# Kernel optimization log

Measured on AMD Instinct MI355X. Metric: run time of the kernel, lower is better.

Reference implementation:

```python
import jax, jax.numpy as jnp
import numpy as np

B, LAT, ADIM, NACT, H = 131072, 64, 16, 9, 128

def setup_inputs() -> dict:
    key = jax.random.key(0)
    ks = jax.random.split(key, 24)
    p = lambda k, shp: (jax.random.normal(k, shp, dtype=jnp.float32) * 0.05)
    return {
        "z_t": jax.random.normal(ks[0], (B, LAT), dtype=jnp.float32),
        "action": jax.random.randint(ks[1], (B,), 0, NACT),
        "hidden": jnp.zeros((1, B, H), dtype=jnp.float32),
        "embed": p(ks[2], (NACT, ADIM)),
        "fuse_W": p(ks[3], (H, LAT + ADIM)), "fuse_b": p(ks[4], (H,)),
        "W_ih": p(ks[5], (3 * H, H)), "W_hh": p(ks[6], (3 * H, H)),
        "b_ih": p(ks[7], (3 * H,)), "b_hh": p(ks[8], (3 * H,)),
        "ns_W1": p(ks[9], (H, H)), "ns_b1": p(ks[10], (H,)),
        "ns_W2": p(ks[11], (LAT, H)), "ns_b2": p(ks[12], (LAT,)),
        "rw_W1": p(ks[13], (H // 2, H)), "rw_b1": p(ks[14], (H // 2,)),
        "rw_W2": p(ks[15], (1, H // 2)), "rw_b2": p(ks[16], (1,)),
        "dn_W1": p(ks[17], (H // 2, H)), "dn_b1": p(ks[18], (H // 2,)),
        "dn_W2": p(ks[19], (1, H // 2)), "dn_b2": p(ks[20], (1,)),
    }

def _mlp2(x, W1, b1, W2, b2):
    return jax.nn.relu(x @ W1.T + b1) @ W2.T + b2

def reference(z_t, action, hidden, embed, fuse_W, fuse_b, W_ih, W_hh, b_ih, b_hh,
              ns_W1, ns_b1, ns_W2, ns_b2, rw_W1, rw_b1, rw_W2, rw_b2,
              dn_W1, dn_b1, dn_W2, dn_b2):
    a_emb = embed[action]                                  # [B, ADIM]
    fused = jnp.concatenate([z_t, a_emb], axis=-1)         # [B, LAT+ADIM]
    x = jax.nn.relu(fused @ fuse_W.T + fuse_b)             # [B, H]
    h0 = hidden[0]                                         # [B, H]
    gi = x @ W_ih.T + b_ih                                 # [B, 3H]
    gh = h0 @ W_hh.T + b_hh                                # [B, 3H]
    Hd = x.shape[-1]
    r = jax.nn.sigmoid(gi[:, :Hd] + gh[:, :Hd])
    zg = jax.nn.sigmoid(gi[:, Hd:2 * Hd] + gh[:, Hd:2 * Hd])
    n = jnp.tanh(gi[:, 2 * Hd:] + r * gh[:, 2 * Hd:])
    h_new = (1.0 - zg) * n + zg * h0                       # [B, H]
    out = h_new
    z_next = _mlp2(out, ns_W1, ns_b1, ns_W2, ns_b2)        # [B, LAT]
    reward = _mlp2(out, rw_W1, rw_b1, rw_W2, rw_b2)        # [B, 1]
    done_logit = _mlp2(out, dn_W1, dn_b1, dn_W2, dn_b2)    # [B, 1]
    return (z_next, reward, done_logit, h_new[None])
```

## Files before the change

kernel.cpp:

```cpp
#include <hip/hip_runtime.h>
#include <hip/hip_bf16.h>
#include <cstddef>
#include <cstdint>

#define BATCH 131072
#define HOFF ((size_t)BATCH * 66)

typedef __attribute__((ext_vector_type(8))) short short8;
typedef __attribute__((ext_vector_type(4))) short short4v;
typedef __attribute__((ext_vector_type(4))) float f32x4;
typedef __attribute__((ext_vector_type(16))) float f32x16;

typedef const __attribute__((address_space(1))) unsigned int* gas_t;
typedef __attribute__((address_space(3))) unsigned int* las_t;

#define WS_G      13312
#define WS_HEAD   117760
#define WS_ELEMS  161280

#define SLOT_A    0
#define SLOT_B    8704
#define STR_BASE  17408

#define MFMA32(a,b,c) __builtin_amdgcn_mfma_f32_32x32x16_bf16((a),(b),(c),0,0,0)

__device__ __forceinline__ short f2bf(float x) {
    __hip_bfloat16 b = __float2bfloat16(x);
    return __builtin_bit_cast(short, b);
}
__device__ __forceinline__ float bf2f(short s) {
    unsigned u = ((unsigned)(unsigned short)s) << 16;
    return __builtin_bit_cast(float, u);
}
__device__ __forceinline__ float fsigmoid(float x) { return __builtin_amdgcn_rcpf(1.0f + __expf(-x)); }
__device__ __forceinline__ float ftanh(float x)    { return 1.0f - 2.0f * __builtin_amdgcn_rcpf(1.0f + __expf(2.0f * x)); }

__device__ __forceinline__ short8 packbf(f32x4 a, f32x4 b) {
    short8 r;
    r[0]=f2bf(a[0]); r[1]=f2bf(a[1]); r[2]=f2bf(a[2]); r[3]=f2bf(a[3]);
    r[4]=f2bf(b[0]); r[5]=f2bf(b[1]); r[6]=f2bf(b[2]); r[7]=f2bf(b[3]);
    return r;
}

template<int NCH>
__device__ __forceinline__ void stage_lds(const short* __restrict__ src, short* dst, int t) {
    constexpr int NP = (NCH + 255) / 256;
    #pragma unroll
    for (int k = 0; k < NP; ++k) {
        int c = t + 256 * k;
        if ((NCH % 256 == 0) || c < NCH)
            __builtin_amdgcn_global_load_lds((gas_t)(const void*)(src + (size_t)c * 8),
                                             (las_t)(void*)(dst + (size_t)c * 8), 16, 0, 0);
    }
}

extern "C" __global__ void prep_weights(const float* __restrict__ fuse_W,
                                        const float* __restrict__ W_ih, const float* __restrict__ W_hh,
                                        const float* __restrict__ ns_W1, const float* __restrict__ ns_W2,
                                        const float* __restrict__ rw_W1, const float* __restrict__ dn_W1,
                                        short* __restrict__ ws) {
    int i = blockIdx.x * 256 + threadIdx.x;
    if (i >= WS_ELEMS) return;
    float v = 0.f;
    if (i < WS_G) {
        int half = i / 6656, e = i % 6656;
        int r = e / 104, k = e % 104;
        if (k < 80) v = fuse_W[(size_t)(half*64 + r)*80 + k];
    } else if (i < WS_HEAD) {
        int rel = i - WS_G;
        int pidx = rel / 8704, e = rel % 8704;
        int q = e / 4352, r = (e % 4352) / 136, k = e % 136;
        if (k < 128) {
            int u = pidx / 3, p = pidx % 3;
            const float* W; int gate;
            if (p == 0)      { W = q ? W_hh : W_ih; gate = 0; }
            else if (p == 1) { W = q ? W_ih : W_hh; gate = 2; }
            else             { W = q ? W_hh : W_ih; gate = 1; }
            v = W[(size_t)(gate*128 + u*32 + r)*128 + k];
        }
    } else {
        int rel = i - WS_HEAD;
        int h = rel / 8704, e = rel % 8704;
        int q = e / 4352, r = (e % 4352) / 136, k = e % 136;
        if (k < 128) {
            const float* W; int rb;
            if (h == 0)      { W = ns_W1; rb = q*32; }
            else if (h == 1) { W = ns_W1; rb = 64 + q*32; }
            else if (h == 2) { W = ns_W2; rb = q*32; }
            else if (h == 3) { W = rw_W1; rb = q*32; }
            else             { W = dn_W1; rb = q*32; }
            v = W[(size_t)(rb + r)*128 + k];
        }
    }
    ws[i] = f2bf(v);
}

#define GRU_R(SB, U) do {                                                                  \
    *(short8*)&S[ln*40 + hb8]      = ha[2*(U)];                                            \
    *(short8*)&S[ln*40 + 16 + hb8] = ha[2*(U)+1];                                          \
    _Pragma("unroll") for (int p = 0; p < 8; ++p) {                                        \
        const int r0 = 2*p, r1 = 2*p + 1;                                                  \
        unsigned a = (unsigned short)S[((r0&3) + 8*(r0>>2) + hr4)*40 + ln];                \
        unsigned b = (unsigned short)S[((r1&3) + 8*(r1>>2) + hr4)*40 + ln];                \
        h0p[p] = a | (b << 16);                                                            \
    }                                                                                      \
    const int cb = (U)*32 + ln;                                                            \
    const float br = b_ih[cb] + b_hh[cb];                                                  \
    f32x16 acc = zz16;                                                                     \
    _Pragma("unroll") for (int kf = 0; kf < 8; ++kf) {                                     \
        const int ko = kf*16 + hb8;                                                        \
        short8 B0 = *(const short8*)&smem[(SB) + ln*136 + ko];                             \
        acc = MFMA32(xa[kf], B0, acc);                                                     \
        short8 B1 = *(const short8*)&smem[(SB) + (32 + ln)*136 + ko];                      \
        acc = MFMA32(ha[kf], B1, acc);                                                     \
    }                                                                                      \
    _Pragma("unroll") for (int reg = 0; reg < 16; ++reg)                                   \
        tmp[reg] = fsigmoid(acc[reg] + br);                                                \
} while (0)

#define GRU_N(SB, U) do {                                                                  \
    const int cb = (U)*32 + ln;                                                            \
    const float bin = b_ih[256 + cb], bhn = b_hh[256 + cb];                                \
    f32x16 acc = zz16;                                                                     \
    _Pragma("unroll") for (int kf = 0; kf < 8; ++kf) {                                     \
        short8 B = *(const short8*)&smem[(SB) + ln*136 + kf*16 + hb8];                     \
        acc = MFMA32(ha[kf], B, acc);                                                      \
    }                                                                                      \
    _Pragma("unroll") for (int reg = 0; reg < 16; ++reg)                                   \
        tmp[reg] = tmp[reg] * (acc[reg] + bhn);                                            \
    acc = zz16;                                                                            \
    _Pragma("unroll") for (int kf = 0; kf < 8; ++kf) {                                     \
        short8 B = *(const short8*)&smem[(SB) + (32 + ln)*136 + kf*16 + hb8];              \
        acc = MFMA32(xa[kf], B, acc);                                                      \
    }                                                                                      \
    _Pragma("unroll") for (int reg = 0; reg < 16; ++reg)                                   \
        tmp[reg] = ftanh(acc[reg] + bin + tmp[reg]);                                       \
} while (0)

#define GRU_Z(SB, U) do {                                                                  \
    const int cb = (U)*32 + ln;                                                            \
    const float bz = b_ih[128 + cb] + b_hh[128 + cb];                                      \
    f32x16 acc = zz16;                                                                     \
    _Pragma("unroll") for (int kf = 0; kf < 8; ++kf) {                                     \
        const int ko = kf*16 + hb8;                                                        \
        short8 B0 = *(const short8*)&smem[(SB) + ln*136 + ko];                             \
        acc = MFMA32(xa[kf], B0, acc);                                                     \
        short8 B1 = *(const short8*)&smem[(SB) + (32 + ln)*136 + ko];                      \
        acc = MFMA32(ha[kf], B1, acc);                                                     \
    }                                                                                      \
    _Pragma("unroll") for (int p = 0; p < 8; ++p) {                                        \
        unsigned hp = h0p[p];                                                              \
        _Pragma("unroll") for (int q = 0; q < 2; ++q) {                                    \
            const int reg = 2*p + q;                                                       \
            float h0v = bf2f((short)(q ? (hp >> 16) : (hp & 0xffffu)));                    \
            float zg = fsigmoid(acc[reg] + bz);                                            \
            S[((reg&3) + 8*(reg>>2) + hr4)*40 + ln] = f2bf((1.f - zg)*tmp[reg] + zg*h0v);  \
        }                                                                                  \
    }                                                                                      \
    hfa[2*(U)]   = *(const short8*)&S[ln*40 + hb8];                                        \
    hfa[2*(U)+1] = *(const short8*)&S[ln*40 + 16 + hb8];                                   \
    store_hnew(U);                                                                         \
} while (0)

#define HEAD32(FRAG, BIASEXPR, SB, Q, RELU) do {                                           \
    f32x16 a = zz16;                                                                       \
    _Pragma("unroll") for (int kf = 0; kf < 8; ++kf) {                                     \
        short8 B = *(const short8*)&smem[(SB) + (Q)*4352 + ln*136 + kf*16 + hb8];          \
        a = MFMA32((FRAG)[kf], B, a);                                                      \
    }                                                                                      \
    const float bb = (BIASEXPR);                                                           \
    _Pragma("unroll") for (int reg = 0; reg < 16; ++reg) {                                 \
        float v = a[reg] + bb;                                                             \
        if (RELU) v = fmaxf(v, 0.f);                                                       \
        S[((reg&3) + 8*(reg>>2) + hr4)*40 + ln] = f2bf(v);                                 \
    }                                                                                      \
} while (0)

extern "C" __global__ __launch_bounds__(256, 1)
void gru_mfma(const float* __restrict__ z_t, const int* __restrict__ action,
              const float* __restrict__ hidden, const float* __restrict__ embed,
              const float* __restrict__ fuse_b,
              const float* __restrict__ b_ih, const float* __restrict__ b_hh,
              const float* __restrict__ ns_b1, const float* __restrict__ ns_b2,
              const float* __restrict__ rw_b1, const float* __restrict__ rw_W2, const float* __restrict__ rw_b2,
              const float* __restrict__ dn_b1, const float* __restrict__ dn_W2, const float* __restrict__ dn_b2,
              const short* __restrict__ ws, float* out)
{
    __shared__ __align__(16) short smem[22528];

    const int t    = threadIdx.x;
    const int lane = t & 63;
    const int w    = t >> 6;
    const int ln   = lane & 31;
    const int hb8  = (lane >> 5) * 8;
    const int hr4  = (lane >> 5) * 4;
    const int R    = blockIdx.x * 128 + w * 32;
    short* const S = &smem[STR_BASE + w * 1280];

    const f32x16 zz16 = {0,0,0,0,0,0,0,0,0,0,0,0,0,0,0,0};

    auto store_hnew = [&](int j2) {
        #pragma unroll
        for (int v = 0; v < 4; ++v) {
            int idx = v*64 + lane;
            int r = idx >> 3, c = (idx & 7) * 4;
            short4v s = *(const short4v*)&S[r*40 + c];
            f32x4 f = { bf2f(s[0]), bf2f(s[1]), bf2f(s[2]), bf2f(s[3]) };
            *(f32x4*)&out[HOFF + (size_t)(R + r)*128 + j2*32 + c] = f;
        }
    };
    auto store_z = [&](int q) {
        #pragma unroll
        for (int v = 0; v < 4; ++v) {
            int idx = v*64 + lane;
            int r = idx >> 3, c = (idx & 7) * 4;
            short4v s = *(const short4v*)&S[r*40 + c];
            f32x4 f = { bf2f(s[0]), bf2f(s[1]), bf2f(s[2]), bf2f(s[3]) };
            *(f32x4*)&out[(size_t)(R + r)*64 + q*32 + c] = f;
        }
    };
    auto hpartial = [&](const float* W2, float acc) -> float {
        int rr = lane & 31;
        #pragma unroll
        for (int kk = 0; kk < 32; kk += 8) {
            short8 s = *(const short8*)&S[rr*40 + kk];
            f32x4 w0 = *(const f32x4*)&W2[kk];
            f32x4 w1 = *(const f32x4*)&W2[kk+4];
            acc += bf2f(s[0])*w0[0] + bf2f(s[1])*w0[1] + bf2f(s[2])*w0[2] + bf2f(s[3])*w0[3]
                 + bf2f(s[4])*w1[0] + bf2f(s[5])*w1[1] + bf2f(s[6])*w1[2] + bf2f(s[7])*w1[3];
        }
        return acc;
    };

    stage_lds<832>(ws, &smem[SLOT_A], t);

    short8 fa[5];
    short8 ha[8];
    {
        const int row = R + ln;
        #pragma unroll
        for (int kf = 0; kf < 4; ++kf) {
            f32x4 p0 = *(const f32x4*)&z_t[(size_t)row*64 + kf*16 + hb8];
            f32x4 p1 = *(const f32x4*)&z_t[(size_t)row*64 + kf*16 + hb8 + 4];
            fa[kf] = packbf(p0, p1);
        }
        int a = action[row];
        f32x4 e0 = *(const f32x4*)&embed[a*16 + hb8];
        f32x4 e1 = *(const f32x4*)&embed[a*16 + hb8 + 4];
        fa[4] = packbf(e0, e1);
        #pragma unroll
        for (int kf = 0; kf < 8; ++kf) {
            f32x4 p0 = *(const f32x4*)&hidden[(size_t)row*128 + kf*16 + hb8];
            f32x4 p1 = *(const f32x4*)&hidden[(size_t)row*128 + kf*16 + hb8 + 4];
            ha[kf] = packbf(p0, p1);
        }
    }

    short8 xa[8], hfa[8];
    f32x16 tmp;
    unsigned h0p[8];

    __syncthreads();
    stage_lds<832>(ws + 6656, &smem[SLOT_B], t);
    #pragma unroll
    for (int n = 0; n < 2; ++n) {
        f32x16 a = zz16;
        #pragma unroll
        for (int kf = 0; kf < 5; ++kf) {
            short8 B = *(const short8*)&smem[SLOT_A + (n*32 + ln)*104 + kf*16 + hb8];
            a = MFMA32(fa[kf], B, a);
        }
        float fb = fuse_b[n*32 + ln];
        #pragma unroll
        for (int reg = 0; reg < 16; ++reg)
            S[((reg&3) + 8*(reg>>2) + hr4)*40 + ln] = f2bf(fmaxf(a[reg] + fb, 0.f));
        xa[2*n]   = *(const short8*)&S[ln*40 + hb8];
        xa[2*n+1] = *(const short8*)&S[ln*40 + 16 + hb8];
    }

    __syncthreads();
    stage_lds<1088>(ws + WS_G + 0*8704, &smem[SLOT_A], t);
    #pragma unroll
    for (int n = 2; n < 4; ++n) {
        f32x16 a = zz16;
        #pragma unroll
        for (int kf = 0; kf < 5; ++kf) {
            short8 B = *(const short8*)&smem[SLOT_B + ((n-2)*32 + ln)*104 + kf*16 + hb8];
            a = MFMA32(fa[kf], B, a);
        }
        float fb = fuse_b[n*32 + ln];
        #pragma unroll
        for (int reg = 0; reg < 16; ++reg)
            S[((reg&3) + 8*(reg>>2) + hr4)*40 + ln] = f2bf(fmaxf(a[reg] + fb, 0.f));
        xa[2*n]   = *(const short8*)&S[ln*40 + hb8];
        xa[2*n+1] = *(const short8*)&S[ln*40 + 16 + hb8];
    }

    __syncthreads();
    stage_lds<1088>(ws + WS_G + 1*8704, &smem[SLOT_B], t);
    GRU_R(SLOT_A, 0);
    __syncthreads();
    stage_lds<1088>(ws + WS_G + 2*8704, &smem[SLOT_A], t);
    GRU_N(SLOT_B, 0);
    __syncthreads();
    stage_lds<1088>(ws + WS_G + 3*8704, &smem[SLOT_B], t);
    GRU_Z(SLOT_A, 0);
    __syncthreads();
    stage_lds<1088>(ws + WS_G + 4*8704, &smem[SLOT_A], t);
    GRU_R(SLOT_B, 1);
    __syncthreads();
    stage_lds<1088>(ws + WS_G + 5*8704, &smem[SLOT_B], t);
    GRU_N(SLOT_A, 1);
    __syncthreads();
    stage_lds<1088>(ws + WS_G + 6*8704, &smem[SLOT_A], t);
    GRU_Z(SLOT_B, 1);
    __syncthreads();
    stage_lds<1088>(ws + WS_G + 7*8704, &smem[SLOT_B], t);
    GRU_R(SLOT_A, 2);
    __syncthreads();
    stage_lds<1088>(ws + WS_G + 8*8704, &smem[SLOT_A], t);
    GRU_N(SLOT_B, 2);
    __syncthreads();
    stage_lds<1088>(ws + WS_G + 9*8704, &smem[SLOT_B], t);
    GRU_Z(SLOT_A, 2);
    __syncthreads();
    stage_lds<1088>(ws + WS_G + 10*8704, &smem[SLOT_A], t);
    GRU_R(SLOT_B, 3);
    __syncthreads();
    stage_lds<1088>(ws + WS_G + 11*8704, &smem[SLOT_B], t);
    GRU_N(SLOT_A, 3);
    __syncthreads();
    stage_lds<1088>(ws + WS_HEAD + 0*8704, &smem[SLOT_A], t);
    GRU_Z(SLOT_B, 3);

    short8 ta[8];
    __syncthreads();
    stage_lds<1088>(ws + WS_HEAD + 1*8704, &smem[SLOT_B], t);
    HEAD32(hfa, ns_b1[ln],      SLOT_A, 0, true);
    ta[0] = *(const short8*)&S[ln*40 + hb8];
    ta[1] = *(const short8*)&S[ln*40 + 16 + hb8];
    HEAD32(hfa, ns_b1[32 + ln], SLOT_A, 1, true);
    ta[2] = *(const short8*)&S[ln*40 + hb8];
    ta[3] = *(const short8*)&S[ln*40 + 16 + hb8];

    __syncthreads();
    stage_lds<1088>(ws + WS_HEAD + 2*8704, &smem[SLOT_A], t);
    HEAD32(hfa, ns_b1[64 + ln], SLOT_B, 0, true);
    ta[4] = *(const short8*)&S[ln*40 + hb8];
    ta[5] = *(const short8*)&S[ln*40 + 16 + hb8];
    HEAD32(hfa, ns_b1[96 + ln], SLOT_B, 1, true);
    ta[6] = *(const short8*)&S[ln*40 + hb8];
    ta[7] = *(const short8*)&S[ln*40 + 16 + hb8];

    __syncthreads();
    stage_lds<1088>(ws + WS_HEAD + 3*8704, &smem[SLOT_B], t);
    HEAD32(ta, ns_b2[ln],      SLOT_A, 0, false);
    store_z(0);
    HEAD32(ta, ns_b2[32 + ln], SLOT_A, 1, false);
    store_z(1);

    __syncthreads();
    stage_lds<1088>(ws + WS_HEAD + 4*8704, &smem[SLOT_A], t);
    float racc = rw_b2[0];
    HEAD32(hfa, rw_b1[ln],      SLOT_B, 0, true);
    racc = hpartial(rw_W2, racc);
    HEAD32(hfa, rw_b1[32 + ln], SLOT_B, 1, true);
    racc = hpartial(rw_W2 + 32, racc);
    if (lane < 32) out[(size_t)BATCH*64 + R + ln] = racc;

    __syncthreads();
    float dacc = dn_b2[0];
    HEAD32(hfa, dn_b1[ln],      SLOT_A, 0, true);
    dacc = hpartial(dn_W2, dacc);
    HEAD32(hfa, dn_b1[32 + ln], SLOT_A, 1, true);
    dacc = hpartial(dn_W2 + 32, dacc);
    if (lane < 32) out[(size_t)BATCH*65 + R + ln] = dacc;
}

extern "C" void kernel_launch(void* const* d_in, const int* in_sizes, int n_in,
                              void* d_out, int out_size, void* d_ws, size_t ws_size,
                              hipStream_t stream) {
    const float* z_t    = (const float*)d_in[0];
    const int*   action = (const int*)  d_in[1];
    const float* hidden = (const float*)d_in[2];
    const float* embed  = (const float*)d_in[3];
    const float* fuse_W = (const float*)d_in[4];
    const float* fuse_b = (const float*)d_in[5];
    const float* W_ih   = (const float*)d_in[6];
    const float* W_hh   = (const float*)d_in[7];
    const float* b_ih   = (const float*)d_in[8];
    const float* b_hh   = (const float*)d_in[9];
    const float* ns_W1  = (const float*)d_in[10];
    const float* ns_b1  = (const float*)d_in[11];
    const float* ns_W2  = (const float*)d_in[12];
    const float* ns_b2  = (const float*)d_in[13];
    const float* rw_W1  = (const float*)d_in[14];
    const float* rw_b1  = (const float*)d_in[15];
    const float* rw_W2  = (const float*)d_in[16];
    const float* rw_b2  = (const float*)d_in[17];
    const float* dn_W1  = (const float*)d_in[18];
    const float* dn_b1  = (const float*)d_in[19];
    const float* dn_W2  = (const float*)d_in[20];
    const float* dn_b2  = (const float*)d_in[21];
    float* out = (float*)d_out;
    short* ws  = (short*)d_ws;

    hipLaunchKernelGGL(prep_weights, dim3((WS_ELEMS + 255) / 256), dim3(256), 0, stream,
                       fuse_W, W_ih, W_hh, ns_W1, ns_W2, rw_W1, dn_W1, ws);

    hipLaunchKernelGGL(gru_mfma, dim3(BATCH / 128), dim3(256), 0, stream,
                       z_t, action, hidden, embed,
                       fuse_b, b_ih, b_hh, ns_b1, ns_b2,
                       rw_b1, rw_W2, rw_b2, dn_b1, dn_W2, dn_b2,
                       ws, out);
}
```

Measured before the change: 82.07 us.

## Write GRU outputs directly from MFMA accumulators and reload h_new via global

Removes the LDS transposes used for h0 extraction, h_new writeback and z_next writeback. h0 values are now read straight from global in the accumulator layout, and h_new and z_next are stored directly from accumulator registers as scalar strided stores. The bf16 operand fragments for the heads are rebuilt by reading h_new back from the output buffer. This cuts LDS traffic and register pressure from the held hfa fragments, but it trades vectorised stores for uncoalesced 4-byte stores and adds global re-reads. The readback also depends on same-thread write visibility, which holds only because each lane reads its own row region after a barrier.

```diff
diff --git a/kernel.cpp b/kernel.cpp
--- a/kernel.cpp
+++ b/kernel.cpp
@@ -96,15 +96,13 @@
 }
 
 #define GRU_R(SB, U) do {                                                                  \
-    *(short8*)&S[ln*40 + hb8]      = ha[2*(U)];                                            \
-    *(short8*)&S[ln*40 + 16 + hb8] = ha[2*(U)+1];                                          \
+    const int cb = (U)*32 + ln;                                                            \
     _Pragma("unroll") for (int p = 0; p < 8; ++p) {                                        \
-        const int r0 = 2*p, r1 = 2*p + 1;                                                  \
-        unsigned a = (unsigned short)S[((r0&3) + 8*(r0>>2) + hr4)*40 + ln];                \
-        unsigned b = (unsigned short)S[((r1&3) + 8*(r1>>2) + hr4)*40 + ln];                \
+        const int r0 = ((2*p)&3) + 8*(p>>1) + hr4;                                         \
+        unsigned a = (unsigned short)f2bf(hidden[(size_t)(R + r0    )*128 + cb]);          \
+        unsigned b = (unsigned short)f2bf(hidden[(size_t)(R + r0 + 1)*128 + cb]);          \
         h0p[p] = a | (b << 16);                                                            \
     }                                                                                      \
-    const int cb = (U)*32 + ln;                                                            \
     const float br = b_ih[cb] + b_hh[cb];                                                  \
     f32x16 acc = zz16;                                                                     \
     _Pragma("unroll") for (int kf = 0; kf < 8; ++kf) {                                     \
@@ -150,16 +148,14 @@
     }                                                                                      \
     _Pragma("unroll") for (int p = 0; p < 8; ++p) {                                        \
         unsigned hp = h0p[p];                                                              \
-        _Pragma("unroll") for (int q = 0; q < 2; ++q) {                                    \
-            const int reg = 2*p + q;                                                       \
-            float h0v = bf2f((short)(q ? (hp >> 16) : (hp & 0xffffu)));                    \
-            float zg = fsigmoid(acc[reg] + bz);                                            \
-            S[((reg&3) + 8*(reg>>2) + hr4)*40 + ln] = f2bf((1.f - zg)*tmp[reg] + zg*h0v);  \
-        }                                                                                  \
-    }                                                                                      \
-    hfa[2*(U)]   = *(const short8*)&S[ln*40 + hb8];                                        \
-    hfa[2*(U)+1] = *(const short8*)&S[ln*40 + 16 + hb8];                                   \
-    store_hnew(U);                                                                         \
+        const int r0 = ((2*p)&3) + 8*(p>>1) + hr4;                                         \
+        {   float h0v = bf2f((short)(hp & 0xffffu));                                       \
+            float zg = fsigmoid(acc[2*p] + bz);                                            \
+            out[HOFF + (size_t)(R + r0)*128 + cb] = (1.f - zg)*tmp[2*p] + zg*h0v; }        \
+        {   float h0v = bf2f((short)(hp >> 16));                                           \
+            float zg = fsigmoid(acc[2*p+1] + bz);                                          \
+            out[HOFF + (size_t)(R + r0 + 1)*128 + cb] = (1.f - zg)*tmp[2*p+1] + zg*h0v; }  \
+    }                                                                                      \
 } while (0)
 
 #define HEAD32(FRAG, BIASEXPR, SB, Q, RELU) do {                                           \
@@ -173,6 +169,19 @@
         float v = a[reg] + bb;                                                             \
         if (RELU) v = fmaxf(v, 0.f);                                                       \
         S[((reg&3) + 8*(reg>>2) + hr4)*40 + ln] = f2bf(v);                                 \
+    }                                                                                      \
+} while (0)
+
+#define HEAD32_ST(FRAG, BIASEXPR, SB, Q, QCOL) do {                                        \
+    f32x16 a = zz16;                                                                       \
+    _Pragma("unroll") for (int kf = 0; kf < 8; ++kf) {                                     \
+        short8 B = *(const short8*)&smem[(SB) + (Q)*4352 + ln*136 + kf*16 + hb8];          \
+        a = MFMA32((FRAG)[kf], B, a);                                                      \
+    }                                                                                      \
+    const float bb = (BIASEXPR);                                                           \
+    _Pragma("unroll") for (int reg = 0; reg < 16; ++reg) {                                 \
+        const int row = (reg&3) + 8*(reg>>2) + hr4;                                        \
+        out[(size_t)(R + row)*64 + (QCOL)*32 + ln] = a[reg] + bb;                          \
     }                                                                                      \
 } while (0)
 
@@ -199,26 +208,6 @@
 
     const f32x16 zz16 = {0,0,0,0,0,0,0,0,0,0,0,0,0,0,0,0};
 
-    auto store_hnew = [&](int j2) {
-        #pragma unroll
-        for (int v = 0; v < 4; ++v) {
-            int idx = v*64 + lane;
-            int r = idx >> 3, c = (idx & 7) * 4;
-            short4v s = *(const short4v*)&S[r*40 + c];
-            f32x4 f = { bf2f(s[0]), bf2f(s[1]), bf2f(s[2]), bf2f(s[3]) };
-            *(f32x4*)&out[HOFF + (size_t)(R + r)*128 + j2*32 + c] = f;
-        }
-    };
-    auto store_z = [&](int q) {
-        #pragma unroll
-        for (int v = 0; v < 4; ++v) {
-            int idx = v*64 + lane;
-            int r = idx >> 3, c = (idx & 7) * 4;
-            short4v s = *(const short4v*)&S[r*40 + c];
-            f32x4 f = { bf2f(s[0]), bf2f(s[1]), bf2f(s[2]), bf2f(s[3]) };
-            *(f32x4*)&out[(size_t)(R + r)*64 + q*32 + c] = f;
-        }
-    };
     auto hpartial = [&](const float* W2, float acc) -> float {
         int rr = lane & 31;
         #pragma unroll
@@ -256,7 +245,7 @@
         }
     }
 
-    short8 xa[8], hfa[8];
+    short8 xa[8];
     f32x16 tmp;
     unsigned h0p[8];
 
@@ -333,9 +322,17 @@
     stage_lds<1088>(ws + WS_HEAD + 0*8704, &smem[SLOT_A], t);
     GRU_Z(SLOT_B, 3);
 
+    __syncthreads();
+    stage_lds<1088>(ws + WS_HEAD + 1*8704, &smem[SLOT_B], t);
+    short8 hfa[8];
+    #pragma unroll
+    for (int kf = 0; kf < 8; ++kf) {
+        const float* p = &out[HOFF + (size_t)(R + ln)*128 + kf*16 + hb8];
+        f32x4 p0 = *(const f32x4*)p;
+        f32x4 p1 = *(const f32x4*)(p + 4);
+        hfa[kf] = packbf(p0, p1);
+    }
     short8 ta[8];
-    __syncthreads();
-    stage_lds<1088>(ws + WS_HEAD + 1*8704, &smem[SLOT_B], t);
     HEAD32(hfa, ns_b1[ln],      SLOT_A, 0, true);
     ta[0] = *(const short8*)&S[ln*40 + hb8];
     ta[1] = *(const short8*)&S[ln*40 + 16 + hb8];
@@ -354,10 +351,8 @@
 
     __syncthreads();
     stage_lds<1088>(ws + WS_HEAD + 3*8704, &smem[SLOT_B], t);
-    HEAD32(ta, ns_b2[ln],      SLOT_A, 0, false);
-    store_z(0);
-    HEAD32(ta, ns_b2[32 + ln], SLOT_A, 1, false);
-    store_z(1);
+    HEAD32_ST(ta, ns_b2[ln],      SLOT_A, 0, 0);
+    HEAD32_ST(ta, ns_b2[32 + ln], SLOT_A, 1, 1);
 
     __syncthreads();
     stage_lds<1088>(ws + WS_HEAD + 4*8704, &smem[SLOT_A], t);
```

Result: slower. 124.9 us (+52.1%).

## Double the block size and stage weights in triple-slot groups with fewer barriers

Applied to the files above, without the earlier changes.

Blocks now have 512 threads (8 waves, 256 rows) instead of 256, and LDS grows to hold the full fuse weights plus six GRU/head weight slots. Weights are staged one gate-group (three slices) at a time, with a single barrier per hidden unit group instead of one per gate. This cuts the barrier count and amortises each weight load over twice as many rows. In exchange it uses about 148KB of LDS, so only one block fits per CU, and it halves the grid to 512 blocks.

```diff
diff --git a/kernel.cpp b/kernel.cpp
--- a/kernel.cpp
+++ b/kernel.cpp
@@ -18,9 +18,8 @@
 #define WS_HEAD   117760
 #define WS_ELEMS  161280
 
-#define SLOT_A    0
-#define SLOT_B    8704
-#define STR_BASE  17408
+#define PSLOT(s)  (13312 + (s)*8704)
+#define STR_BASE  65536
 
 #define MFMA32(a,b,c) __builtin_amdgcn_mfma_f32_32x32x16_bf16((a),(b),(c),0,0,0)
 
@@ -44,11 +43,11 @@
 
 template<int NCH>
 __device__ __forceinline__ void stage_lds(const short* __restrict__ src, short* dst, int t) {
-    constexpr int NP = (NCH + 255) / 256;
+    constexpr int NP = (NCH + 511) / 512;
     #pragma unroll
     for (int k = 0; k < NP; ++k) {
-        int c = t + 256 * k;
-        if ((NCH % 256 == 0) || c < NCH)
+        int c = t + 512 * k;
+        if ((NCH % 512 == 0) || c < NCH)
             __builtin_amdgcn_global_load_lds((gas_t)(const void*)(src + (size_t)c * 8),
                                              (las_t)(void*)(dst + (size_t)c * 8), 16, 0, 0);
     }
@@ -63,9 +62,8 @@
     if (i >= WS_ELEMS) return;
     float v = 0.f;
     if (i < WS_G) {
-        int half = i / 6656, e = i % 6656;
-        int r = e / 104, k = e % 104;
-        if (k < 80) v = fuse_W[(size_t)(half*64 + r)*80 + k];
+        int r = i / 104, k = i % 104;
+        if (k < 80) v = fuse_W[(size_t)r*80 + k];
     } else if (i < WS_HEAD) {
         int rel = i - WS_G;
         int pidx = rel / 8704, e = rel % 8704;
@@ -111,7 +109,7 @@
         const int ko = kf*16 + hb8;                                                        \
         short8 B0 = *(const short8*)&smem[(SB) + ln*136 + ko];                             \
         acc = MFMA32(xa[kf], B0, acc);                                                     \
-        short8 B1 = *(const short8*)&smem[(SB) + (32 + ln)*136 + ko];                      \
+        short8 B1 = *(const short8*)&smem[(SB) + 4352 + ln*136 + ko];                      \
         acc = MFMA32(ha[kf], B1, acc);                                                     \
     }                                                                                      \
     _Pragma("unroll") for (int reg = 0; reg < 16; ++reg)                                   \
@@ -130,7 +128,7 @@
         tmp[reg] = tmp[reg] * (acc[reg] + bhn);                                            \
     acc = zz16;                                                                            \
     _Pragma("unroll") for (int kf = 0; kf < 8; ++kf) {                                     \
-        short8 B = *(const short8*)&smem[(SB) + (32 + ln)*136 + kf*16 + hb8];              \
+        short8 B = *(const short8*)&smem[(SB) + 4352 + ln*136 + kf*16 + hb8];              \
         acc = MFMA32(xa[kf], B, acc);                                                      \
     }                                                                                      \
     _Pragma("unroll") for (int reg = 0; reg < 16; ++reg)                                   \
@@ -145,7 +143,7 @@
         const int ko = kf*16 + hb8;                                                        \
         short8 B0 = *(const short8*)&smem[(SB) + ln*136 + ko];                             \
         acc = MFMA32(xa[kf], B0, acc);                                                     \
-        short8 B1 = *(const short8*)&smem[(SB) + (32 + ln)*136 + ko];                      \
+        short8 B1 = *(const short8*)&smem[(SB) + 4352 + ln*136 + ko];                      \
         acc = MFMA32(ha[kf], B1, acc);                                                     \
     }                                                                                      \
     _Pragma("unroll") for (int p = 0; p < 8; ++p) {                                        \
@@ -162,10 +160,10 @@
     store_hnew(U);                                                                         \
 } while (0)
 
-#define HEAD32(FRAG, BIASEXPR, SB, Q, RELU) do {                                           \
+#define HEAD32(FRAG, BIASEXPR, UB, RELU) do {                                              \
     f32x16 a = zz16;                                                                       \
     _Pragma("unroll") for (int kf = 0; kf < 8; ++kf) {                                     \
-        short8 B = *(const short8*)&smem[(SB) + (Q)*4352 + ln*136 + kf*16 + hb8];          \
+        short8 B = *(const short8*)&smem[(UB) + ln*136 + kf*16 + hb8];                     \
         a = MFMA32((FRAG)[kf], B, a);                                                      \
     }                                                                                      \
     const float bb = (BIASEXPR);                                                           \
@@ -176,7 +174,7 @@
     }                                                                                      \
 } while (0)
 
-extern "C" __global__ __launch_bounds__(256, 1)
+extern "C" __global__ __launch_bounds__(512, 1)
 void gru_mfma(const float* __restrict__ z_t, const int* __restrict__ action,
               const float* __restrict__ hidden, const float* __restrict__ embed,
               const float* __restrict__ fuse_b,
@@ -186,7 +184,7 @@
               const float* __restrict__ dn_b1, const float* __restrict__ dn_W2, const float* __restrict__ dn_b2,
               const short* __restrict__ ws, float* out)
 {
-    __shared__ __align__(16) short smem[22528];
+    __shared__ __align__(16) short smem[75776];
 
     const int t    = threadIdx.x;
     const int lane = t & 63;
@@ -194,7 +192,7 @@
     const int ln   = lane & 31;
     const int hb8  = (lane >> 5) * 8;
     const int hr4  = (lane >> 5) * 4;
-    const int R    = blockIdx.x * 128 + w * 32;
+    const int R    = blockIdx.x * 256 + w * 32;
     short* const S = &smem[STR_BASE + w * 1280];
 
     const f32x16 zz16 = {0,0,0,0,0,0,0,0,0,0,0,0,0,0,0,0};
@@ -232,7 +230,8 @@
         return acc;
     };
 
-    stage_lds<832>(ws, &smem[SLOT_A], t);
+    stage_lds<1664>(ws, &smem[0], t);
+    stage_lds<6528>(ws + WS_G, &smem[PSLOT(0)], t);
 
     short8 fa[5];
     short8 ha[8];
@@ -261,13 +260,13 @@
     unsigned h0p[8];
 
     __syncthreads();
-    stage_lds<832>(ws + 6656, &smem[SLOT_B], t);
+
     #pragma unroll
-    for (int n = 0; n < 2; ++n) {
+    for (int n = 0; n < 4; ++n) {
         f32x16 a = zz16;
         #pragma unroll
         for (int kf = 0; kf < 5; ++kf) {
-            short8 B = *(const short8*)&smem[SLOT_A + (n*32 + ln)*104 + kf*16 + hb8];
+            short8 B = *(const short8*)&smem[(n*32 + ln)*104 + kf*16 + hb8];
             a = MFMA32(fa[kf], B, a);
         }
         float fb = fuse_b[n*32 + ln];
@@ -278,102 +277,61 @@
         xa[2*n+1] = *(const short8*)&S[ln*40 + 16 + hb8];
     }
 
-    __syncthreads();
-    stage_lds<1088>(ws + WS_G + 0*8704, &smem[SLOT_A], t);
-    #pragma unroll
-    for (int n = 2; n < 4; ++n) {
-        f32x16 a = zz16;
-        #pragma unroll
-        for (int kf = 0; kf < 5; ++kf) {
-            short8 B = *(const short8*)&smem[SLOT_B + ((n-2)*32 + ln)*104 + kf*16 + hb8];
-            a = MFMA32(fa[kf], B, a);
-        }
-        float fb = fuse_b[n*32 + ln];
-        #pragma unroll
-        for (int reg = 0; reg < 16; ++reg)
-            S[((reg&3) + 8*(reg>>2) + hr4)*40 + ln] = f2bf(fmaxf(a[reg] + fb, 0.f));
-        xa[2*n]   = *(const short8*)&S[ln*40 + hb8];
-        xa[2*n+1] = *(const short8*)&S[ln*40 + 16 + hb8];
-    }
-
-    __syncthreads();
-    stage_lds<1088>(ws + WS_G + 1*8704, &smem[SLOT_B], t);
-    GRU_R(SLOT_A, 0);
-    __syncthreads();
-    stage_lds<1088>(ws + WS_G + 2*8704, &smem[SLOT_A], t);
-    GRU_N(SLOT_B, 0);
-    __syncthreads();
-    stage_lds<1088>(ws + WS_G + 3*8704, &smem[SLOT_B], t);
-    GRU_Z(SLOT_A, 0);
-    __syncthreads();
-    stage_lds<1088>(ws + WS_G + 4*8704, &smem[SLOT_A], t);
-    GRU_R(SLOT_B, 1);
-    __syncthreads();
-    stage_lds<1088>(ws + WS_G + 5*8704, &smem[SLOT_B], t);
-    GRU_N(SLOT_A, 1);
-    __syncthreads();
-    stage_lds<1088>(ws + WS_G + 6*8704, &smem[SLOT_A], t);
-    GRU_Z(SLOT_B, 1);
-    __syncthreads();
-    stage_lds<1088>(ws + WS_G + 7*8704, &smem[SLOT_B], t);
-    GRU_R(SLOT_A, 2);
-    __syncthreads();
-    stage_lds<1088>(ws + WS_G + 8*8704, &smem[SLOT_A], t);
-    GRU_N(SLOT_B, 2);
-    __syncthreads();
-    stage_lds<1088>(ws + WS_G + 9*8704, &smem[SLOT_B], t);
-    GRU_Z(SLOT_A, 2);
-    __syncthreads();
-    stage_lds<1088>(ws + WS_G + 10*8704, &smem[SLOT_A], t);
-    GRU_R(SLOT_B, 3);
-    __syncthreads();
-    stage_lds<1088>(ws + WS_G + 11*8704, &smem[SLOT_B], t);
-    GRU_N(SLOT_A, 3);
-    __syncthreads();
-    stage_lds<1088>(ws + WS_HEAD + 0*8704, &smem[SLOT_A], t);
-    GRU_Z(SLOT_B, 3);
+    GRU_R(PSLOT(0), 0);
+    GRU_N(PSLOT(1), 0);
+    GRU_Z(PSLOT(2), 0);
+
+    __syncthreads();
+    stage_lds<3264>(ws + WS_G + 6*8704, &smem[PSLOT(0)], t);
+
+    GRU_R(PSLOT(3), 1);
+    GRU_N(PSLOT(4), 1);
+    GRU_Z(PSLOT(5), 1);
+
+    __syncthreads();
+    stage_lds<3264>(ws + WS_G + 9*8704, &smem[PSLOT(3)], t);
+
+    GRU_R(PSLOT(0), 2);
+    GRU_N(PSLOT(1), 2);
+    GRU_Z(PSLOT(2), 2);
+
+    __syncthreads();
+    stage_lds<3264>(ws + WS_HEAD, &smem[PSLOT(0)], t);
+
+    GRU_R(PSLOT(3), 3);
+    GRU_N(PSLOT(4), 3);
+    GRU_Z(PSLOT(5), 3);
+
+    __syncthreads();
+    stage_lds<2176>(ws + WS_HEAD + 3*8704, &smem[PSLOT(3)], t);
 
     short8 ta[8];
-    __syncthreads();
-    stage_lds<1088>(ws + WS_HEAD + 1*8704, &smem[SLOT_B], t);
-    HEAD32(hfa, ns_b1[ln],      SLOT_A, 0, true);
+    HEAD32(hfa, ns_b1[ln],      PSLOT(0),        true);
     ta[0] = *(const short8*)&S[ln*40 + hb8];
     ta[1] = *(const short8*)&S[ln*40 + 16 + hb8];
-    HEAD32(hfa, ns_b1[32 + ln], SLOT_A, 1, true);
+    HEAD32(hfa, ns_b1[32 + ln], PSLOT(0) + 4352, true);
     ta[2] = *(const short8*)&S[ln*40 + hb8];
     ta[3] = *(const short8*)&S[ln*40 + 16 + hb8];
-
-    __syncthreads();
-    stage_lds<1088>(ws + WS_HEAD + 2*8704, &smem[SLOT_A], t);
-    HEAD32(hfa, ns_b1[64 + ln], SLOT_B, 0, true);
+    HEAD32(hfa, ns_b1[64 + ln], PSLOT(1),        true);
     ta[4] = *(const short8*)&S[ln*40 + hb8];
     ta[5] = *(const short8*)&S[ln*40 + 16 + hb8];
-    HEAD32(hfa, ns_b1[96 + ln], SLOT_B, 1, true);
+    HEAD32(hfa, ns_b1[96 + ln], PSLOT(1) + 4352, true);
     ta[6] = *(const short8*)&S[ln*40 + hb8];
     ta[7] = *(const short8*)&S[ln*40 + 16 + hb8];
 
-    __syncthreads();
-    stage_lds<1088>(ws + WS_HEAD + 3*8704, &smem[SLOT_B], t);
-    HEAD32(ta, ns_b2[ln],      SLOT_A, 0, false);
-    store_z(0);
-    HEAD32(ta, ns_b2[32 + ln], SLOT_A, 1, false);
-    store_z(1);
-
-    __syncthreads();
-    stage_lds<1088>(ws + WS_HEAD + 4*8704, &smem[SLOT_A], t);
+    HEAD32(ta, ns_b2[ln],      PSLOT(2),        false); store_z(0);
+    HEAD32(ta, ns_b2[32 + ln], PSLOT(2) + 4352, false); store_z(1);
+
+    __syncthreads();
+
     float racc = rw_b2[0];
-    HEAD32(hfa, rw_b1[ln],      SLOT_B, 0, true);
-    racc = hpartial(rw_W2, racc);
-    HEAD32(hfa, rw_b1[32 + ln], SLOT_B, 1, true);
-    racc = hpartial(rw_W2 + 32, racc);
+    HEAD32(hfa, rw_b1[ln],      PSLOT(3),        true); racc = hpartial(rw_W2, racc);
+    HEAD32(hfa, rw_b1[32 + ln], PSLOT(3) + 4352, true); racc = hpartial(rw_W2 + 32, racc);
     if (lane < 32) out[(size_t)BATCH*64 + R + ln] = racc;
 
-    __syncthreads();
     float dacc = dn_b2[0];
-    HEAD32(hfa, dn_b1[ln],      SLOT_A, 0, true);
-    dacc = hpartial(dn_W2, dacc);
-    HEAD32(hfa, dn_b1[32 + ln], SLOT_A, 1, true);
-    dacc = hpartial(dn_W2 + 32, dacc);
+    HEAD32(hfa, dn_b1[ln],      PSLOT(4),        true); dacc = hpartial(dn_W2, dacc);
+    HEAD32(hfa, dn_b1[32 + ln], PSLOT(4) + 4352, true); dacc = hpartial(dn_W2 + 32, dacc);
     if (lane < 32) out[(size_t)BATCH*65 + R + ln] = dacc;
 }
 
@@ -408,7 +366,7 @@
     hipLaunchKernelGGL(prep_weights, dim3((WS_ELEMS + 255) / 256), dim3(256), 0, stream,
                        fuse_W, W_ih, W_hh, ns_W1, ns_W2, rw_W1, dn_W1, ws);
 
-    hipLaunchKernelGGL(gru_mfma, dim3(BATCH / 128), dim3(256), 0, stream,
+    hipLaunchKernelGGL(gru_mfma, dim3(BATCH / 256), dim3(512), 0, stream,
                        z_t, action, hidden, embed,
                        fuse_b, b_ih, b_hh, ns_b1, ns_b2,
                        rw_b1, rw_W2, rw_b2, dn_b1, dn_W2, dn_b2,
```

New measurement: 78.82 us. 1.04x faster.
